# Performance work log

Measured on AMD Instinct MI355X. Metric: run time of the kernel, lower is better.

## Reference

```python
import jax, jax.numpy as jnp
import numpy as np

B, F, H, M, T = 4096, 256, 256, 3, 30
IN0 = 2 + F  # GRU layer-0 input: concat(current_pos[2], context[F])


def setup_inputs() -> dict:
    key = jax.random.key(0)
    ks = jax.random.split(key, 15)
    s = 0.05
    rn = lambda k, shp: jax.random.normal(k, shp, jnp.float32) * s
    return dict(
        context=jax.random.normal(ks[0], (B, F), jnp.float32),
        mp_w1=rn(ks[1], (64, F)), mp_b1=rn(ks[2], (64,)),
        mp_w2=rn(ks[3], (M, 64)), mp_b2=rn(ks[4], (M,)),
        w_ih0=rn(ks[5], (M, 3 * H, IN0)), w_hh0=rn(ks[6], (M, 3 * H, H)),
        b_ih0=rn(ks[7], (M, 3 * H)), b_hh0=rn(ks[8], (M, 3 * H)),
        w_ih1=rn(ks[9], (M, 3 * H, H)), w_hh1=rn(ks[10], (M, 3 * H, H)),
        b_ih1=rn(ks[11], (M, 3 * H)), b_hh1=rn(ks[12], (M, 3 * H)),
        out_w=rn(ks[13], (M, 2, H)), out_b=rn(ks[14], (M, 2)),
        num_future_steps=T,
    )


def _gru_cell(x, h, w_ih, w_hh, b_ih, b_hh):
    # PyTorch GRU cell, gate order (r, z, n)
    gx = x @ w_ih.T + b_ih  # (B, 3H)
    gh = h @ w_hh.T + b_hh  # (B, 3H)
    xr, xz, xn = jnp.split(gx, 3, axis=-1)
    hr, hz, hn = jnp.split(gh, 3, axis=-1)
    r = jax.nn.sigmoid(xr + hr)
    z = jax.nn.sigmoid(xz + hz)
    n = jnp.tanh(xn + r * hn)
    return (1.0 - z) * n + z * h


def reference(context, mp_w1, mp_b1, mp_w2, mp_b2,
              w_ih0, w_hh0, b_ih0, b_hh0,
              w_ih1, w_hh1, b_ih1, b_hh1,
              out_w, out_b, num_future_steps):
    mode_logits = jax.nn.relu(context @ mp_w1.T + mp_b1) @ mp_w2.T + mp_b2
    mode_probs = jax.nn.softmax(mode_logits, axis=-1)  # (B, M)

    def decode_mode(wi0, wh0, bi0, bh0, wi1, wh1, bi1, bh1, ow, ob):
        def step(carry, _):
            h0, h1, pos = carry
            x = jnp.concatenate([pos, context], axis=-1)  # (B, 2+F)
            h0n = _gru_cell(x, h0, wi0, wh0, bi0, bh0)
            h1n = _gru_cell(h0n, h1, wi1, wh1, bi1, bh1)
            delta = h1n @ ow.T + ob  # (B, 2)
            return (h0n, h1n, delta), delta

        pos0 = jnp.zeros((context.shape[0], 2), context.dtype)
        # hidden = context.unsqueeze(0).repeat(2,1,1): both layers init to context
        (_, _, _), deltas = jax.lax.scan(step, (context, context, pos0), None,
                                          length=num_future_steps)
        # deltas: (T, B, 2) -> (B, T, 2), cumulative sum over time
        return jnp.cumsum(deltas.transpose(1, 0, 2), axis=1)

    trajs = jax.vmap(decode_mode)(w_ih0, w_hh0, b_ih0, b_hh0,
                                  w_ih1, w_hh1, b_ih1, b_hh1,
                                  out_w, out_b)  # (M, B, T, 2)
    trajectories = trajs.transpose(1, 0, 2, 3)  # (B, M, T, 2)
    return trajectories, mode_probs
```

## Files before the change

kernel.cpp:

```cpp
#include <hip/hip_runtime.h>


typedef __attribute__((ext_vector_type(8))) short bf16x8;
typedef __attribute__((ext_vector_type(4))) short short4n;
typedef __attribute__((ext_vector_type(4))) float f32x4;

__device__ __forceinline__ short f2bf(float f) {
    unsigned u = __builtin_bit_cast(unsigned, f);
    unsigned r = (u + 0x7fffu + ((u >> 16) & 1u)) >> 16;
    return (short)r;
}
__device__ __forceinline__ float bf2f(short s) {
    unsigned u = ((unsigned)(unsigned short)s) << 16;
    return __builtin_bit_cast(float, u);
}
__device__ __forceinline__ float fast_sigmoid(float x) {
    x = fminf(fmaxf(x, -30.f), 30.f);
    float e = __builtin_amdgcn_exp2f(x * -1.442695041f);
    return __builtin_amdgcn_rcpf(1.f + e);
}
__device__ __forceinline__ float fast_tanh(float x) {
    x = fminf(fmaxf(x, -15.f), 15.f);
    float e = __builtin_amdgcn_exp2f(x * -2.885390082f);
    return (1.f - e) * __builtin_amdgcn_rcpf(1.f + e);
}

__global__ void prep_kernel(const float* __restrict__ w_ih0,
                            const float* __restrict__ w_hh0,
                            const float* __restrict__ w_ih1,
                            const float* __restrict__ w_hh1,
                            short* __restrict__ ws) {
    int bid = blockIdx.x;
    int L = threadIdx.x;
    const float* src;
    int srcRowLen, colBase, m, w, ks, t;
    if (bid < 1152) {
        int idx = bid, mw = idx / 48, blk = idx % 48;
        m = mw / 8; w = mw % 8;
        if (blk < 32) { ks = blk >> 2; t = blk & 3; }
        else { int q = blk - 32; ks = q >> 1; t = 4 + (q & 1); }
        src = w_hh0 + (size_t)m * 768 * 256; srcRowLen = 256; colBase = 0;
    } else if (bid < 3456) {
        int idx = bid - 1152, mw = idx / 96, blk = idx % 96;
        m = mw / 8; w = mw % 8;
        int half;
        if (blk < 64) { half = blk >> 5; ks = (blk >> 2) & 7; t = blk & 3; }
        else { int q = blk - 64; half = q >> 4; ks = (q >> 1) & 7; t = 4 + (q & 1); }
        src = (half ? w_hh1 : w_ih1) + (size_t)m * 768 * 256;
        srcRowLen = 256; colBase = 0;
    } else {
        int idx = bid - 3456, mw = idx / 48, blk = idx % 48;
        m = mw / 8; w = mw % 8; ks = blk / 6; t = blk % 6;
        src = w_ih0 + (size_t)m * 768 * 258; srcRowLen = 258; colBase = 2;
    }
    int row = (t >> 1) * 256 + 32 * w + (t & 1) * 16 + (L & 15);
    int col0 = colBase + ks * 32 + (L >> 4) * 8;
    short* dst = ws + (size_t)bid * 512 + L * 8;
    const float* s = src + (size_t)row * srcRowLen + col0;
#pragma unroll
    for (int j = 0; j < 8; ++j) dst[j] = f2bf(s[j]);
}

__global__ __launch_bounds__(256) void modeprobs_kernel(
    const float* __restrict__ ctx, const float* __restrict__ w1,
    const float* __restrict__ b1, const float* __restrict__ w2,
    const float* __restrict__ b2, float* __restrict__ out,
    long probs_off) {
    __shared__ float w1s[64 * 256];
    int tid = threadIdx.x;
    int j = tid & 63;
    int rsub = tid >> 6;
#pragma unroll
    for (int i = 0; i < 64; ++i) w1s[tid + i * 256] = w1[tid + i * 256];
    float b1v = b1[j];
    float w2v0 = w2[j], w2v1 = w2[64 + j], w2v2 = w2[128 + j];
    float b20 = b2[0], b21 = b2[1], b22 = b2[2];
    __syncthreads();
    for (int c = 0; c < 16; ++c) {
        int brow = blockIdx.x * 64 + c * 4 + rsub;
        const float* crow = ctx + (size_t)brow * 256;
        float accv = b1v;
#pragma unroll 8
        for (int k = 0; k < 256; ++k) {
            int kk = (k + j) & 255;
            accv += w1s[j * 256 + kk] * crow[kk];
        }
        float h = fmaxf(accv, 0.f);
        float l0 = h * w2v0, l1 = h * w2v1, l2 = h * w2v2;
#pragma unroll
        for (int s = 1; s < 64; s <<= 1) {
            l0 += __shfl_xor(l0, s);
            l1 += __shfl_xor(l1, s);
            l2 += __shfl_xor(l2, s);
        }
        if (j == 0) {
            l0 += b20; l1 += b21; l2 += b22;
            float mx = fmaxf(l0, fmaxf(l1, l2));
            float e0 = __builtin_amdgcn_exp2f((l0 - mx) * 1.442695041f);
            float e1 = __builtin_amdgcn_exp2f((l1 - mx) * 1.442695041f);
            float e2 = __builtin_amdgcn_exp2f((l2 - mx) * 1.442695041f);
            float inv = 1.f / (e0 + e1 + e2);
            out[probs_off + (size_t)brow * 3 + 0] = e0 * inv;
            out[probs_off + (size_t)brow * 3 + 1] = e1 * inv;
            out[probs_off + (size_t)brow * 3 + 2] = e2 * inv;
        }
    }
}

__global__ __launch_bounds__(512, 2) void decoder_gxc2(
    const float* __restrict__ context,
    const float* __restrict__ w_ih0_f,
    const float* __restrict__ b_ih0, const float* __restrict__ b_hh0,
    const float* __restrict__ b_ih1, const float* __restrict__ b_hh1,
    const float* __restrict__ out_w, const float* __restrict__ out_b,
    short* ws, float* __restrict__ out,
    const int* __restrict__ pT, int ntiles) {
    __shared__ short h0s[64 * 264];
    __shared__ short h1s[64 * 264];
    __shared__ short gxcrz[8 * 16 * 256];
    __shared__ float posD[128];
    __shared__ float owl[512];
    __shared__ short cwp0h[768], cwp1h[768];
    __shared__ float cbA[512];
    __shared__ float cbXn[256];
    __shared__ float cbh0n[256];
    __shared__ float cb1A[512];
    __shared__ float cb1X[256];
    __shared__ float cb1H[256];

    const int bid = blockIdx.x;
    const int xcd = bid & 7, slot = bid >> 3;
    int mode, xl, nx;
    if (xcd < 3)      { mode = 0; xl = xcd;     nx = 3; }
    else if (xcd < 6) { mode = 1; xl = xcd - 3; nx = 3; }
    else              { mode = 2; xl = xcd - 6; nx = 2; }
    const int g = slot * nx + xl;
    if (g >= ntiles) return;
    const int m = mode;
    const int b0 = g * 64;
    const int wk = m * ntiles + g;

    const int T = *pT;
    const int tid = threadIdx.x;
    const int lane = tid & 63, w = tid >> 6;
    const int lr = lane & 15, quad = lane >> 4;

    if (tid < 128) posD[tid] = 0.f;
    owl[tid] = out_w[m * 512 + tid];
    if (tid < 512) {
        cbA[tid] = b_ih0[m * 768 + tid] + b_hh0[m * 768 + tid];
        cb1A[tid] = b_ih1[m * 768 + tid] + b_hh1[m * 768 + tid];
    }
    if (tid < 256) {
        cbXn[tid] = b_ih0[m * 768 + 512 + tid];
        cbh0n[tid] = b_hh0[m * 768 + 512 + tid];
        cb1X[tid] = b_ih1[m * 768 + 512 + tid];
        cb1H[tid] = b_hh1[m * 768 + 512 + tid];
    }
    for (int cc = tid; cc < 768; cc += 512) {
        cwp0h[cc] = f2bf(w_ih0_f[((size_t)m * 768 + cc) * 258 + 0]);
        cwp1h[cc] = f2bf(w_ih0_f[((size_t)m * 768 + cc) * 258 + 1]);
    }
#pragma unroll
    for (int i = 0; i < 32; ++i) {
        int idx = tid + i * 512;
        int r = idx >> 8, k = idx & 255;
        short v = f2bf(context[(size_t)(b0 + r) * 256 + k]);
        h0s[r * 264 + k] = v;
        h1s[r * 264 + k] = v;
    }
    const float ob0v = out_b[m * 2 + 0], ob1v = out_b[m * 2 + 1];

    const short* p0w = ws + ((size_t)(m * 8 + w) * 48) * 512 + lane * 8;
    const short* p1w = ws + (size_t)1152 * 512 + ((size_t)(m * 8 + w) * 96) * 512 + lane * 8;
    const short* pcw = ws + (size_t)3456 * 512 + ((size_t)(m * 8 + w) * 48) * 512 + lane * 8;

    short* gxw = ws + (size_t)4608 * 512 +
                 ((size_t)(wk * 8 + w) * 8) * 256 + lane * 4;
    short* grz = gxcrz + (w * 16) * 256 + lane * 4;

    const int cA = 32 * w + lr;
    const int cB = 32 * w + 16 + lr;

    __syncthreads();

    {
        f32x4 arz[4][4], axn[2][4];
#pragma unroll
        for (int rt = 0; rt < 4; ++rt)
#pragma unroll
            for (int r = 0; r < 4; ++r) {
#pragma unroll
                for (int t = 0; t < 4; ++t) {
                    int c = (t >> 1) * 256 + ((t & 1) ? cB : cA);
                    arz[t][rt][r] = cbA[c];
                }
#pragma unroll
                for (int nt = 0; nt < 2; ++nt)
                    axn[nt][rt][r] = cbXn[nt ? cB : cA];
            }
        const short* bpc = pcw;
#pragma unroll 1
        for (int ks = 0; ks < 8; ++ks) {
            bf16x8 ac[4];
#pragma unroll
            for (int rt = 0; rt < 4; ++rt)
                ac[rt] = *reinterpret_cast<const bf16x8*>(
                    h0s + (rt * 16 + lr) * 264 + ks * 32 + quad * 8);
#pragma unroll
            for (int t = 0; t < 4; ++t) {
                bf16x8 b = *reinterpret_cast<const bf16x8*>(bpc + t * 512);
#pragma unroll
                for (int rt = 0; rt < 4; ++rt)
                    arz[t][rt] = __builtin_amdgcn_mfma_f32_16x16x32_bf16(
                        ac[rt], b, arz[t][rt], 0, 0, 0);
            }
#pragma unroll
            for (int nt = 0; nt < 2; ++nt) {
                bf16x8 b = *reinterpret_cast<const bf16x8*>(bpc + (4 + nt) * 512);
#pragma unroll
                for (int rt = 0; rt < 4; ++rt)
                    axn[nt][rt] = __builtin_amdgcn_mfma_f32_16x16x32_bf16(
                        ac[rt], b, axn[nt][rt], 0, 0, 0);
            }
            bpc += 6 * 512;
        }
#pragma unroll
        for (int t = 0; t < 4; ++t)
#pragma unroll
            for (int rt = 0; rt < 4; ++rt) {
                short4n pk;
#pragma unroll
                for (int r = 0; r < 4; ++r) pk[r] = f2bf(arz[t][rt][r]);
                *reinterpret_cast<short4n*>(grz + (t * 4 + rt) * 256) = pk;
            }
#pragma unroll
        for (int nt = 0; nt < 2; ++nt)
#pragma unroll
            for (int rt = 0; rt < 4; ++rt) {
                short4n pk;
#pragma unroll
                for (int r = 0; r < 4; ++r) pk[r] = f2bf(axn[nt][rt][r]);
                *reinterpret_cast<short4n*>(gxw + (nt * 4 + rt) * 256) = pk;
            }
        asm volatile("s_waitcnt vmcnt(0)" ::: "memory");
    }
    __syncthreads();

    float cum0 = 0.f, cum1 = 0.f;

    for (int st = 0; st < T; ++st) {
        {
            int gxo = 0;
            asm volatile("" : "+v"(gxo));
            const short* gq = gxw + gxo;

            f32x4 arz[4][4], axn[2][4], ahn[2][4];
#pragma unroll
            for (int t = 0; t < 4; ++t) {
                const int c = (t >> 1) * 256 + ((t & 1) ? cB : cA);
                const float w0 = bf2f(cwp0h[c]), w1 = bf2f(cwp1h[c]);
#pragma unroll
                for (int rt = 0; rt < 4; ++rt) {
                    short4n v = *reinterpret_cast<const short4n*>(
                        grz + (t * 4 + rt) * 256);
#pragma unroll
                    for (int r = 0; r < 4; ++r) {
                        int row = rt * 16 + quad * 4 + r;
                        arz[t][rt][r] = bf2f(v[r]) + posD[row * 2] * w0 +
                                        posD[row * 2 + 1] * w1;
                    }
                }
            }
#pragma unroll
            for (int nt = 0; nt < 2; ++nt) {
                const int cn = nt ? cB : cA;
                const float w0 = bf2f(cwp0h[512 + cn]);
                const float w1 = bf2f(cwp1h[512 + cn]);
                const float bh = cbh0n[cn];
#pragma unroll
                for (int rt = 0; rt < 4; ++rt) {
                    short4n v = *reinterpret_cast<const short4n*>(
                        gq + (nt * 4 + rt) * 256);
#pragma unroll
                    for (int r = 0; r < 4; ++r) {
                        int row = rt * 16 + quad * 4 + r;
                        axn[nt][rt][r] = bf2f(v[r]) + posD[row * 2] * w0 +
                                         posD[row * 2 + 1] * w1;
                        ahn[nt][rt][r] = bh;
                    }
                }
            }
            const short* b0r = p0w;
            const short* b0n = p0w + 32 * 512;
#pragma unroll 1
            for (int ks = 0; ks < 8; ++ks) {
                bf16x8 ah[4];
#pragma unroll
                for (int rt = 0; rt < 4; ++rt)
                    ah[rt] = *reinterpret_cast<const bf16x8*>(
                        h0s + (rt * 16 + lr) * 264 + ks * 32 + quad * 8);
#pragma unroll
                for (int t = 0; t < 4; ++t) {
                    bf16x8 b = *reinterpret_cast<const bf16x8*>(b0r + t * 512);
#pragma unroll
                    for (int rt = 0; rt < 4; ++rt)
                        arz[t][rt] = __builtin_amdgcn_mfma_f32_16x16x32_bf16(
                            ah[rt], b, arz[t][rt], 0, 0, 0);
                }
#pragma unroll
                for (int nt = 0; nt < 2; ++nt) {
                    bf16x8 b = *reinterpret_cast<const bf16x8*>(b0n + nt * 512);
#pragma unroll
                    for (int rt = 0; rt < 4; ++rt)
                        ahn[nt][rt] = __builtin_amdgcn_mfma_f32_16x16x32_bf16(
                            ah[rt], b, ahn[nt][rt], 0, 0, 0);
                }
                b0r += 4 * 512;
                b0n += 2 * 512;
            }
            __syncthreads();
#pragma unroll
            for (int nt = 0; nt < 2; ++nt) {
                int col = nt ? cB : cA;
#pragma unroll
                for (int rt = 0; rt < 4; ++rt)
#pragma unroll
                    for (int r = 0; r < 4; ++r) {
                        int row = rt * 16 + quad * 4 + r;
                        float rr = fast_sigmoid(arz[nt][rt][r]);
                        float zz = fast_sigmoid(arz[2 + nt][rt][r]);
                        float nn =
                            fast_tanh(axn[nt][rt][r] + rr * ahn[nt][rt][r]);
                        float hold = bf2f(h0s[row * 264 + col]);
                        h0s[row * 264 + col] = f2bf((1.f - zz) * nn + zz * hold);
                    }
            }
        }
        __syncthreads();

        {
            f32x4 arz[4][4], axn[2][4], ahn[2][4];
#pragma unroll
            for (int rt = 0; rt < 4; ++rt)
#pragma unroll
                for (int r = 0; r < 4; ++r) {
#pragma unroll
                    for (int t = 0; t < 4; ++t) {
                        int c = (t >> 1) * 256 + ((t & 1) ? cB : cA);
                        arz[t][rt][r] = cb1A[c];
                    }
#pragma unroll
                    for (int nt = 0; nt < 2; ++nt) {
                        int cn = nt ? cB : cA;
                        axn[nt][rt][r] = cb1X[cn];
                        ahn[nt][rt][r] = cb1H[cn];
                    }
                }
            const short* bq0 = p1w;
            const short* bq1 = p1w + 32 * 512;
            const short* bx = p1w + 64 * 512;
            const short* bh = p1w + 80 * 512;
#pragma unroll 1
            for (int ks = 0; ks < 8; ++ks) {
                bf16x8 a0[4], a1[4];
#pragma unroll
                for (int rt = 0; rt < 4; ++rt) {
                    a0[rt] = *reinterpret_cast<const bf16x8*>(
                        h0s + (rt * 16 + lr) * 264 + ks * 32 + quad * 8);
                    a1[rt] = *reinterpret_cast<const bf16x8*>(
                        h1s + (rt * 16 + lr) * 264 + ks * 32 + quad * 8);
                }
#pragma unroll
                for (int t = 0; t < 4; ++t) {
                    bf16x8 b = *reinterpret_cast<const bf16x8*>(bq0 + t * 512);
#pragma unroll
                    for (int rt = 0; rt < 4; ++rt)
                        arz[t][rt] = __builtin_amdgcn_mfma_f32_16x16x32_bf16(
                            a0[rt], b, arz[t][rt], 0, 0, 0);
                }
#pragma unroll
                for (int nt = 0; nt < 2; ++nt) {
                    bf16x8 b = *reinterpret_cast<const bf16x8*>(bx + nt * 512);
#pragma unroll
                    for (int rt = 0; rt < 4; ++rt)
                        axn[nt][rt] = __builtin_amdgcn_mfma_f32_16x16x32_bf16(
                            a0[rt], b, axn[nt][rt], 0, 0, 0);
                }
#pragma unroll
                for (int t = 0; t < 4; ++t) {
                    bf16x8 b = *reinterpret_cast<const bf16x8*>(bq1 + t * 512);
#pragma unroll
                    for (int rt = 0; rt < 4; ++rt)
                        arz[t][rt] = __builtin_amdgcn_mfma_f32_16x16x32_bf16(
                            a1[rt], b, arz[t][rt], 0, 0, 0);
                }
#pragma unroll
                for (int nt = 0; nt < 2; ++nt) {
                    bf16x8 b = *reinterpret_cast<const bf16x8*>(bh + nt * 512);
#pragma unroll
                    for (int rt = 0; rt < 4; ++rt)
                        ahn[nt][rt] = __builtin_amdgcn_mfma_f32_16x16x32_bf16(
                            a1[rt], b, ahn[nt][rt], 0, 0, 0);
                }
                bq0 += 4 * 512;
                bq1 += 4 * 512;
                bx += 2 * 512;
                bh += 2 * 512;
            }
            __syncthreads();
#pragma unroll
            for (int nt = 0; nt < 2; ++nt) {
                int col = nt ? cB : cA;
#pragma unroll
                for (int rt = 0; rt < 4; ++rt)
#pragma unroll
                    for (int r = 0; r < 4; ++r) {
                        int row = rt * 16 + quad * 4 + r;
                        float rr = fast_sigmoid(arz[nt][rt][r]);
                        float zz = fast_sigmoid(arz[2 + nt][rt][r]);
                        float nn =
                            fast_tanh(axn[nt][rt][r] + rr * ahn[nt][rt][r]);
                        float hold = bf2f(h1s[row * 264 + col]);
                        h1s[row * 264 + col] = f2bf((1.f - zz) * nn + zz * hold);
                    }
            }
        }
        __syncthreads();

        {
            int brow = tid >> 3, p = tid & 7;
            float d0 = 0.f, d1 = 0.f;
#pragma unroll
            for (int j = 0; j < 4; ++j) {
                int cb = ((p + brow) & 7) * 8 + j * 64;
                bf16x8 hv8 = *reinterpret_cast<const bf16x8*>(h1s + brow * 264 + cb);
#pragma unroll
                for (int i = 0; i < 8; ++i) {
                    float hv = bf2f(hv8[i]);
                    d0 += hv * owl[cb + i];
                    d1 += hv * owl[256 + cb + i];
                }
            }
            d0 += __shfl_xor(d0, 1); d0 += __shfl_xor(d0, 2); d0 += __shfl_xor(d0, 4);
            d1 += __shfl_xor(d1, 1); d1 += __shfl_xor(d1, 2); d1 += __shfl_xor(d1, 4);
            d0 += ob0v;
            d1 += ob1v;
            if (p == 0) {
                cum0 += d0;
                cum1 += d1;
                size_t o = (((size_t)(b0 + brow) * 3 + m) * (size_t)T + st) * 2;
                out[o] = cum0;
                out[o + 1] = cum1;
                posD[brow * 2] = d0;
                posD[brow * 2 + 1] = d1;
            }
        }
        __syncthreads();
    }
}

__global__ __launch_bounds__(512, 2) void decoder_base(
    const float* __restrict__ context,
    const float* __restrict__ w_ih0_f,
    const float* __restrict__ b_ih0, const float* __restrict__ b_hh0,
    const float* __restrict__ b_ih1, const float* __restrict__ b_hh1,
    const float* __restrict__ out_w, const float* __restrict__ out_b,
    const short* __restrict__ ws, float* __restrict__ out,
    const int* __restrict__ pT, int ntiles) {
    __shared__ short ctxS[64 * 264];
    __shared__ short h0a[64 * 264], h0b[64 * 264];
    __shared__ short h1s[64 * 264];
    __shared__ float posD[128];
    __shared__ float owl[512];
    __shared__ float cwp0[768], cwp1[768];
    __shared__ float cbA[512];
    __shared__ float cbXn[256];
    __shared__ float cbh0n[256];
    __shared__ float cb1A[512];
    __shared__ float cb1X[256];
    __shared__ float cb1H[256];

    const int bid = blockIdx.x;
    const int xcd = bid & 7, slot = bid >> 3;
    int mode, xl, nx;
    if (xcd < 3)      { mode = 0; xl = xcd;     nx = 3; }
    else if (xcd < 6) { mode = 1; xl = xcd - 3; nx = 3; }
    else              { mode = 2; xl = xcd - 6; nx = 2; }
    const int g = slot * nx + xl;
    if (g >= ntiles) return;
    const int m = mode;
    const int b0 = g * 64;

    const int T = *pT;
    const int tid = threadIdx.x;
    const int lane = tid & 63, w = tid >> 6;
    const int lr = lane & 15, quad = lane >> 4;

    if (tid < 128) posD[tid] = 0.f;
    owl[tid] = out_w[m * 512 + tid];
    if (tid < 512) {
        cbA[tid] = b_ih0[m * 768 + tid] + b_hh0[m * 768 + tid];
        cb1A[tid] = b_ih1[m * 768 + tid] + b_hh1[m * 768 + tid];
    }
    if (tid < 256) {
        cbXn[tid] = b_ih0[m * 768 + 512 + tid];
        cbh0n[tid] = b_hh0[m * 768 + 512 + tid];
        cb1X[tid] = b_ih1[m * 768 + 512 + tid];
        cb1H[tid] = b_hh1[m * 768 + 512 + tid];
    }
    for (int c = tid; c < 768; c += 512) {
        cwp0[c] = w_ih0_f[((size_t)m * 768 + c) * 258 + 0];
        cwp1[c] = w_ih0_f[((size_t)m * 768 + c) * 258 + 1];
    }
#pragma unroll
    for (int i = 0; i < 32; ++i) {
        int idx = tid + i * 512;
        int r = idx >> 8, k = idx & 255;
        short v = f2bf(context[(size_t)(b0 + r) * 256 + k]);
        ctxS[r * 264 + k] = v;
        h0a[r * 264 + k] = v;
        h1s[r * 264 + k] = v;
    }
    const float ob0v = out_b[m * 2 + 0], ob1v = out_b[m * 2 + 1];

    const short* p0w = ws + ((size_t)(m * 8 + w) * 48) * 512 + lane * 8;
    const short* p1w = ws + (size_t)1152 * 512 + ((size_t)(m * 8 + w) * 96) * 512 + lane * 8;
    const short* pcw = ws + (size_t)3456 * 512 + ((size_t)(m * 8 + w) * 48) * 512 + lane * 8;

    const int cA = 32 * w + lr;
    const int cB = 32 * w + 16 + lr;

    __syncthreads();

    float cum0 = 0.f, cum1 = 0.f;

    for (int st = 0; st < T; ++st) {
        const short* h0c = (st & 1) ? h0b : h0a;
        short* h0n_ = (st & 1) ? h0a : h0b;

        {
            f32x4 arz[4][4], axn[2][4], ahn[2][4];
#pragma unroll
            for (int rt = 0; rt < 4; ++rt)
#pragma unroll
                for (int r = 0; r < 4; ++r) {
                    int row = rt * 16 + quad * 4 + r;
                    float px = posD[row * 2], py = posD[row * 2 + 1];
#pragma unroll
                    for (int t = 0; t < 4; ++t) {
                        int c = (t >> 1) * 256 + ((t & 1) ? cB : cA);
                        arz[t][rt][r] = cbA[c] + px * cwp0[c] + py * cwp1[c];
                    }
#pragma unroll
                    for (int nt = 0; nt < 2; ++nt) {
                        int cn = nt ? cB : cA;
                        axn[nt][rt][r] = cbXn[cn] + px * cwp0[512 + cn] +
                                         py * cwp1[512 + cn];
                        ahn[nt][rt][r] = cbh0n[cn];
                    }
                }
            const short* bpc = pcw;
            const short* bp0rz = p0w;
            const short* bp0n = p0w + 32 * 512;
#pragma unroll 1
            for (int ks = 0; ks < 8; ++ks) {
                bf16x8 ac[4], ah[4];
#pragma unroll
                for (int rt = 0; rt < 4; ++rt) {
                    ac[rt] = *reinterpret_cast<const bf16x8*>(
                        ctxS + (rt * 16 + lr) * 264 + ks * 32 + quad * 8);
                    ah[rt] = *reinterpret_cast<const bf16x8*>(
                        h0c + (rt * 16 + lr) * 264 + ks * 32 + quad * 8);
                }
#pragma unroll
                for (int t = 0; t < 4; ++t) {
                    bf16x8 b = *reinterpret_cast<const bf16x8*>(bpc + t * 512);
#pragma unroll
                    for (int rt = 0; rt < 4; ++rt)
                        arz[t][rt] = __builtin_amdgcn_mfma_f32_16x16x32_bf16(
                            ac[rt], b, arz[t][rt], 0, 0, 0);
                }
#pragma unroll
                for (int nt = 0; nt < 2; ++nt) {
                    bf16x8 b = *reinterpret_cast<const bf16x8*>(bpc + (4 + nt) * 512);
#pragma unroll
                    for (int rt = 0; rt < 4; ++rt)
                        axn[nt][rt] = __builtin_amdgcn_mfma_f32_16x16x32_bf16(
                            ac[rt], b, axn[nt][rt], 0, 0, 0);
                }
#pragma unroll
                for (int t = 0; t < 4; ++t) {
                    bf16x8 b = *reinterpret_cast<const bf16x8*>(bp0rz + t * 512);
#pragma unroll
                    for (int rt = 0; rt < 4; ++rt)
                        arz[t][rt] = __builtin_amdgcn_mfma_f32_16x16x32_bf16(
                            ah[rt], b, arz[t][rt], 0, 0, 0);
                }
#pragma unroll
                for (int nt = 0; nt < 2; ++nt) {
                    bf16x8 b = *reinterpret_cast<const bf16x8*>(bp0n + nt * 512);
#pragma unroll
                    for (int rt = 0; rt < 4; ++rt)
                        ahn[nt][rt] = __builtin_amdgcn_mfma_f32_16x16x32_bf16(
                            ah[rt], b, ahn[nt][rt], 0, 0, 0);
                }
                bpc += 6 * 512;
                bp0rz += 4 * 512;
                bp0n += 2 * 512;
            }
#pragma unroll
            for (int nt = 0; nt < 2; ++nt) {
                int col = nt ? cB : cA;
#pragma unroll
                for (int rt = 0; rt < 4; ++rt)
#pragma unroll
                    for (int r = 0; r < 4; ++r) {
                        int row = rt * 16 + quad * 4 + r;
                        float rr = fast_sigmoid(arz[nt][rt][r]);
                        float zz = fast_sigmoid(arz[2 + nt][rt][r]);
                        float nn =
                            fast_tanh(axn[nt][rt][r] + rr * ahn[nt][rt][r]);
                        float hold = bf2f(h0c[row * 264 + col]);
                        h0n_[row * 264 + col] = f2bf((1.f - zz) * nn + zz * hold);
                    }
            }
        }
        __syncthreads();

        {
            f32x4 arz[4][4], axn[2][4], ahn[2][4];
#pragma unroll
            for (int rt = 0; rt < 4; ++rt)
#pragma unroll
                for (int r = 0; r < 4; ++r) {
#pragma unroll
                    for (int t = 0; t < 4; ++t) {
                        int c = (t >> 1) * 256 + ((t & 1) ? cB : cA);
                        arz[t][rt][r] = cb1A[c];
                    }
#pragma unroll
                    for (int nt = 0; nt < 2; ++nt) {
                        int cn = nt ? cB : cA;
                        axn[nt][rt][r] = cb1X[cn];
                        ahn[nt][rt][r] = cb1H[cn];
                    }
                }
            const short* bq0 = p1w;
            const short* bq1 = p1w + 32 * 512;
            const short* bx = p1w + 64 * 512;
            const short* bh = p1w + 80 * 512;
#pragma unroll 1
            for (int ks = 0; ks < 8; ++ks) {
                bf16x8 a0[4], a1[4];
#pragma unroll
                for (int rt = 0; rt < 4; ++rt) {
                    a0[rt] = *reinterpret_cast<const bf16x8*>(
                        h0n_ + (rt * 16 + lr) * 264 + ks * 32 + quad * 8);
                    a1[rt] = *reinterpret_cast<const bf16x8*>(
                        h1s + (rt * 16 + lr) * 264 + ks * 32 + quad * 8);
                }
#pragma unroll
                for (int t = 0; t < 4; ++t) {
                    bf16x8 b = *reinterpret_cast<const bf16x8*>(bq0 + t * 512);
#pragma unroll
                    for (int rt = 0; rt < 4; ++rt)
                        arz[t][rt] = __builtin_amdgcn_mfma_f32_16x16x32_bf16(
                            a0[rt], b, arz[t][rt], 0, 0, 0);
                }
#pragma unroll
                for (int nt = 0; nt < 2; ++nt) {
                    bf16x8 b = *reinterpret_cast<const bf16x8*>(bx + nt * 512);
#pragma unroll
                    for (int rt = 0; rt < 4; ++rt)
                        axn[nt][rt] = __builtin_amdgcn_mfma_f32_16x16x32_bf16(
                            a0[rt], b, axn[nt][rt], 0, 0, 0);
                }
#pragma unroll
                for (int t = 0; t < 4; ++t) {
                    bf16x8 b = *reinterpret_cast<const bf16x8*>(bq1 + t * 512);
#pragma unroll
                    for (int rt = 0; rt < 4; ++rt)
                        arz[t][rt] = __builtin_amdgcn_mfma_f32_16x16x32_bf16(
                            a1[rt], b, arz[t][rt], 0, 0, 0);
                }
#pragma unroll
                for (int nt = 0; nt < 2; ++nt) {
                    bf16x8 b = *reinterpret_cast<const bf16x8*>(bh + nt * 512);
#pragma unroll
                    for (int rt = 0; rt < 4; ++rt)
                        ahn[nt][rt] = __builtin_amdgcn_mfma_f32_16x16x32_bf16(
                            a1[rt], b, ahn[nt][rt], 0, 0, 0);
                }
                bq0 += 4 * 512;
                bq1 += 4 * 512;
                bx += 2 * 512;
                bh += 2 * 512;
            }
            __syncthreads();
#pragma unroll
            for (int nt = 0; nt < 2; ++nt) {
                int col = nt ? cB : cA;
#pragma unroll
                for (int rt = 0; rt < 4; ++rt)
#pragma unroll
                    for (int r = 0; r < 4; ++r) {
                        int row = rt * 16 + quad * 4 + r;
                        float rr = fast_sigmoid(arz[nt][rt][r]);
                        float zz = fast_sigmoid(arz[2 + nt][rt][r]);
                        float nn =
                            fast_tanh(axn[nt][rt][r] + rr * ahn[nt][rt][r]);
                        float hold = bf2f(h1s[row * 264 + col]);
                        h1s[row * 264 + col] = f2bf((1.f - zz) * nn + zz * hold);
                    }
            }
        }
        __syncthreads();

        {
            int brow = tid >> 3, p = tid & 7;
            float d0 = 0.f, d1 = 0.f;
#pragma unroll
            for (int j = 0; j < 4; ++j) {
                int cb = ((p + brow) & 7) * 8 + j * 64;
                bf16x8 hv8 = *reinterpret_cast<const bf16x8*>(h1s + brow * 264 + cb);
#pragma unroll
                for (int i = 0; i < 8; ++i) {
                    float hv = bf2f(hv8[i]);
                    d0 += hv * owl[cb + i];
                    d1 += hv * owl[256 + cb + i];
                }
            }
            d0 += __shfl_xor(d0, 1); d0 += __shfl_xor(d0, 2); d0 += __shfl_xor(d0, 4);
            d1 += __shfl_xor(d1, 1); d1 += __shfl_xor(d1, 2); d1 += __shfl_xor(d1, 4);
            d0 += ob0v;
            d1 += ob1v;
            if (p == 0) {
                cum0 += d0;
                cum1 += d1;
                size_t o = (((size_t)(b0 + brow) * 3 + m) * (size_t)T + st) * 2;
                out[o] = cum0;
                out[o + 1] = cum1;
                posD[brow * 2] = d0;
                posD[brow * 2 + 1] = d1;
            }
        }
        __syncthreads();
    }
}

extern "C" void kernel_launch(void* const* d_in, const int* in_sizes, int n_in,
                              void* d_out, int out_size, void* d_ws, size_t ws_size,
                              hipStream_t stream) {
    const float* context = (const float*)d_in[0];
    const float* mp_w1 = (const float*)d_in[1];
    const float* mp_b1 = (const float*)d_in[2];
    const float* mp_w2 = (const float*)d_in[3];
    const float* mp_b2 = (const float*)d_in[4];
    const float* w_ih0 = (const float*)d_in[5];
    const float* w_hh0 = (const float*)d_in[6];
    const float* b_ih0 = (const float*)d_in[7];
    const float* b_hh0 = (const float*)d_in[8];
    const float* w_ih1 = (const float*)d_in[9];
    const float* w_hh1 = (const float*)d_in[10];
    const float* b_ih1 = (const float*)d_in[11];
    const float* b_hh1 = (const float*)d_in[12];
    const float* out_w = (const float*)d_in[13];
    const float* out_b = (const float*)d_in[14];
    const int* pT = (const int*)d_in[15];
    float* out = (float*)d_out;
    short* ws = (short*)d_ws;

    const int B = in_sizes[0] / 256;
    const int ntiles = B / 64;
    const long probs_off = (long)out_size - (long)B * 3;

    prep_kernel<<<4608, 64, 0, stream>>>(w_ih0, w_hh0, w_ih1, w_hh1, ws);
    modeprobs_kernel<<<B / 64, 256, 0, stream>>>(context, mp_w1, mp_b1, mp_w2,
                                                 mp_b2, out, probs_off);
    const int nslots = (ntiles + 1) / 2;

    const size_t needed =
        ((size_t)4608 * 512 + (size_t)3 * ntiles * 8 * 8 * 256) * sizeof(short);
    if (ws_size >= needed) {
        decoder_gxc2<<<8 * nslots, 512, 0, stream>>>(
            context, w_ih0, b_ih0, b_hh0, b_ih1, b_hh1, out_w, out_b, ws, out,
            pT, ntiles);
    } else {
        decoder_base<<<8 * nslots, 512, 0, stream>>>(
            context, w_ih0, b_ih0, b_hh0, b_ih1, b_hh1, out_w, out_b, ws, out,
            pT, ntiles);
    }
}
```

Measured before the change: 876.2 us.

## Split decoder into 32-row tiles with 256-thread blocks, two column groups per wave

The decoder moves from 64-row batch tiles with 8 waves to 32-row tiles with 4 waves, each wave now handling two 32-column gate groups. Work items (mode, tile) are assigned to blocks contiguously per XCD lane, replacing the hard-coded mode-to-XCD mapping. This doubles the block count (384 vs 192), which should fill more CUs on a 256-CU part and cut the length of the serial recurrence chain per block. In exchange, each weight fragment is reused across fewer rows, so per-block weight traffic relative to useful work roughly doubles, and register pressure per wave rises.

```diff
diff --git a/kernel.cpp b/kernel.cpp
--- a/kernel.cpp
+++ b/kernel.cpp
@@ -107,18 +107,18 @@
     }
 }
 
-__global__ __launch_bounds__(512, 2) void decoder_gxc2(
+__global__ __launch_bounds__(256, 2) void decoder_gxc32(
     const float* __restrict__ context,
     const float* __restrict__ w_ih0_f,
     const float* __restrict__ b_ih0, const float* __restrict__ b_hh0,
     const float* __restrict__ b_ih1, const float* __restrict__ b_hh1,
     const float* __restrict__ out_w, const float* __restrict__ out_b,
     short* ws, float* __restrict__ out,
-    const int* __restrict__ pT, int ntiles) {
-    __shared__ short h0s[64 * 264];
-    __shared__ short h1s[64 * 264];
-    __shared__ short gxcrz[8 * 16 * 256];
-    __shared__ float posD[128];
+    const int* __restrict__ pT, int tilesPerMode, int nwork) {
+    __shared__ short h0s[32 * 264];
+    __shared__ short h1s[32 * 264];
+    __shared__ short gxcrz[8 * 8 * 256];
+    __shared__ float posD[64];
     __shared__ float owl[512];
     __shared__ short cwp0h[768], cwp1h[768];
     __shared__ float cbA[512];
@@ -128,121 +128,139 @@
     __shared__ float cb1X[256];
     __shared__ float cb1H[256];
 
-    const int bid = blockIdx.x;
-    const int xcd = bid & 7, slot = bid >> 3;
-    int mode, xl, nx;
-    if (xcd < 3)      { mode = 0; xl = xcd;     nx = 3; }
-    else if (xcd < 6) { mode = 1; xl = xcd - 3; nx = 3; }
-    else              { mode = 2; xl = xcd - 6; nx = 2; }
-    const int g = slot * nx + xl;
-    if (g >= ntiles) return;
-    const int m = mode;
-    const int b0 = g * 64;
-    const int wk = m * ntiles + g;
+    const int lane8 = blockIdx.x & 7, slot = blockIdx.x >> 3;
+    const int q = nwork >> 3, r8 = nwork & 7;
+    int start, cnt;
+    if (lane8 < r8) { cnt = q + 1; start = lane8 * (q + 1); }
+    else            { cnt = q;     start = r8 * (q + 1) + (lane8 - r8) * q; }
+    if (slot >= cnt) return;
+    const int wk = start + slot;
+    const int m = wk / tilesPerMode;
+    const int b0 = (wk - m * tilesPerMode) * 32;
 
     const int T = *pT;
     const int tid = threadIdx.x;
     const int lane = tid & 63, w = tid >> 6;
     const int lr = lane & 15, quad = lane >> 4;
 
-    if (tid < 128) posD[tid] = 0.f;
+    if (tid < 64) posD[tid] = 0.f;
     owl[tid] = out_w[m * 512 + tid];
-    if (tid < 512) {
-        cbA[tid] = b_ih0[m * 768 + tid] + b_hh0[m * 768 + tid];
-        cb1A[tid] = b_ih1[m * 768 + tid] + b_hh1[m * 768 + tid];
-    }
-    if (tid < 256) {
-        cbXn[tid] = b_ih0[m * 768 + 512 + tid];
-        cbh0n[tid] = b_hh0[m * 768 + 512 + tid];
-        cb1X[tid] = b_ih1[m * 768 + 512 + tid];
-        cb1H[tid] = b_hh1[m * 768 + 512 + tid];
-    }
-    for (int cc = tid; cc < 768; cc += 512) {
+    owl[256 + tid] = out_w[m * 512 + 256 + tid];
+    cbA[tid] = b_ih0[m * 768 + tid] + b_hh0[m * 768 + tid];
+    cbA[256 + tid] = b_ih0[m * 768 + 256 + tid] + b_hh0[m * 768 + 256 + tid];
+    cb1A[tid] = b_ih1[m * 768 + tid] + b_hh1[m * 768 + tid];
+    cb1A[256 + tid] = b_ih1[m * 768 + 256 + tid] + b_hh1[m * 768 + 256 + tid];
+    cbXn[tid] = b_ih0[m * 768 + 512 + tid];
+    cbh0n[tid] = b_hh0[m * 768 + 512 + tid];
+    cb1X[tid] = b_ih1[m * 768 + 512 + tid];
+    cb1H[tid] = b_hh1[m * 768 + 512 + tid];
+    for (int cc = tid; cc < 768; cc += 256) {
         cwp0h[cc] = f2bf(w_ih0_f[((size_t)m * 768 + cc) * 258 + 0]);
         cwp1h[cc] = f2bf(w_ih0_f[((size_t)m * 768 + cc) * 258 + 1]);
     }
 #pragma unroll
     for (int i = 0; i < 32; ++i) {
-        int idx = tid + i * 512;
-        int r = idx >> 8, k = idx & 255;
-        short v = f2bf(context[(size_t)(b0 + r) * 256 + k]);
-        h0s[r * 264 + k] = v;
-        h1s[r * 264 + k] = v;
+        int idx = tid + i * 256;
+        int rr = idx >> 8, k = idx & 255;
+        short v = f2bf(context[(size_t)(b0 + rr) * 256 + k]);
+        h0s[rr * 264 + k] = v;
+        h1s[rr * 264 + k] = v;
     }
     const float ob0v = out_b[m * 2 + 0], ob1v = out_b[m * 2 + 1];
 
-    const short* p0w = ws + ((size_t)(m * 8 + w) * 48) * 512 + lane * 8;
-    const short* p1w = ws + (size_t)1152 * 512 + ((size_t)(m * 8 + w) * 96) * 512 + lane * 8;
-    const short* pcw = ws + (size_t)3456 * 512 + ((size_t)(m * 8 + w) * 48) * 512 + lane * 8;
-
-    short* gxw = ws + (size_t)4608 * 512 +
-                 ((size_t)(wk * 8 + w) * 8) * 256 + lane * 4;
-    short* grz = gxcrz + (w * 16) * 256 + lane * 4;
-
-    const int cA = 32 * w + lr;
-    const int cB = 32 * w + 16 + lr;
+    const short* p0B[2];
+    const short* p1B[2];
+    const short* pcB[2];
+    short* gxB[2];
+#pragma unroll
+    for (int g2 = 0; g2 < 2; ++g2) {
+        const int wg = 2 * w + g2;
+        p0B[g2] = ws + ((size_t)(m * 8 + wg) * 48) * 512 + lane * 8;
+        p1B[g2] = ws + (size_t)1152 * 512 + ((size_t)(m * 8 + wg) * 96) * 512 + lane * 8;
+        pcB[g2] = ws + (size_t)3456 * 512 + ((size_t)(m * 8 + wg) * 48) * 512 + lane * 8;
+        gxB[g2] = ws + (size_t)4608 * 512 +
+                  ((size_t)(wk * 8 + wg) * 4) * 256 + lane * 4;
+    }
 
     __syncthreads();
 
     {
-        f32x4 arz[4][4], axn[2][4];
-#pragma unroll
-        for (int rt = 0; rt < 4; ++rt)
-#pragma unroll
-            for (int r = 0; r < 4; ++r) {
-#pragma unroll
-                for (int t = 0; t < 4; ++t) {
-                    int c = (t >> 1) * 256 + ((t & 1) ? cB : cA);
-                    arz[t][rt][r] = cbA[c];
-                }
-#pragma unroll
-                for (int nt = 0; nt < 2; ++nt)
-                    axn[nt][rt][r] = cbXn[nt ? cB : cA];
-            }
-        const short* bpc = pcw;
+        f32x4 arz[2][4][2], axn[2][2][2];
+#pragma unroll
+        for (int g2 = 0; g2 < 2; ++g2) {
+            const int cbase = 32 * (2 * w + g2) + lr;
+#pragma unroll
+            for (int t = 0; t < 4; ++t) {
+                const int c = (t >> 1) * 256 + cbase + (t & 1) * 16;
+                const float bb = cbA[c];
+#pragma unroll
+                for (int rt = 0; rt < 2; ++rt)
+#pragma unroll
+                    for (int r = 0; r < 4; ++r) arz[g2][t][rt][r] = bb;
+            }
+#pragma unroll
+            for (int nt = 0; nt < 2; ++nt) {
+                const float bx = cbXn[cbase + nt * 16];
+#pragma unroll
+                for (int rt = 0; rt < 2; ++rt)
+#pragma unroll
+                    for (int r = 0; r < 4; ++r) axn[g2][nt][rt][r] = bx;
+            }
+        }
+        const short* bpc0 = pcB[0];
+        const short* bpc1 = pcB[1];
 #pragma unroll 1
         for (int ks = 0; ks < 8; ++ks) {
-            bf16x8 ac[4];
-#pragma unroll
-            for (int rt = 0; rt < 4; ++rt)
+            bf16x8 ac[2];
+#pragma unroll
+            for (int rt = 0; rt < 2; ++rt)
                 ac[rt] = *reinterpret_cast<const bf16x8*>(
                     h0s + (rt * 16 + lr) * 264 + ks * 32 + quad * 8);
 #pragma unroll
-            for (int t = 0; t < 4; ++t) {
-                bf16x8 b = *reinterpret_cast<const bf16x8*>(bpc + t * 512);
-#pragma unroll
-                for (int rt = 0; rt < 4; ++rt)
-                    arz[t][rt] = __builtin_amdgcn_mfma_f32_16x16x32_bf16(
-                        ac[rt], b, arz[t][rt], 0, 0, 0);
-            }
-#pragma unroll
-            for (int nt = 0; nt < 2; ++nt) {
-                bf16x8 b = *reinterpret_cast<const bf16x8*>(bpc + (4 + nt) * 512);
-#pragma unroll
-                for (int rt = 0; rt < 4; ++rt)
-                    axn[nt][rt] = __builtin_amdgcn_mfma_f32_16x16x32_bf16(
-                        ac[rt], b, axn[nt][rt], 0, 0, 0);
-            }
-            bpc += 6 * 512;
-        }
-#pragma unroll
-        for (int t = 0; t < 4; ++t)
-#pragma unroll
-            for (int rt = 0; rt < 4; ++rt) {
-                short4n pk;
-#pragma unroll
-                for (int r = 0; r < 4; ++r) pk[r] = f2bf(arz[t][rt][r]);
-                *reinterpret_cast<short4n*>(grz + (t * 4 + rt) * 256) = pk;
-            }
-#pragma unroll
-        for (int nt = 0; nt < 2; ++nt)
-#pragma unroll
-            for (int rt = 0; rt < 4; ++rt) {
-                short4n pk;
-#pragma unroll
-                for (int r = 0; r < 4; ++r) pk[r] = f2bf(axn[nt][rt][r]);
-                *reinterpret_cast<short4n*>(gxw + (nt * 4 + rt) * 256) = pk;
-            }
+            for (int g2 = 0; g2 < 2; ++g2) {
+                const short* bpc = g2 ? bpc1 : bpc0;
+#pragma unroll
+                for (int t = 0; t < 4; ++t) {
+                    bf16x8 b = *reinterpret_cast<const bf16x8*>(bpc + t * 512);
+#pragma unroll
+                    for (int rt = 0; rt < 2; ++rt)
+                        arz[g2][t][rt] = __builtin_amdgcn_mfma_f32_16x16x32_bf16(
+                            ac[rt], b, arz[g2][t][rt], 0, 0, 0);
+                }
+#pragma unroll
+                for (int nt = 0; nt < 2; ++nt) {
+                    bf16x8 b = *reinterpret_cast<const bf16x8*>(bpc + (4 + nt) * 512);
+#pragma unroll
+                    for (int rt = 0; rt < 2; ++rt)
+                        axn[g2][nt][rt] = __builtin_amdgcn_mfma_f32_16x16x32_bf16(
+                            ac[rt], b, axn[g2][nt][rt], 0, 0, 0);
+                }
+            }
+            bpc0 += 6 * 512;
+            bpc1 += 6 * 512;
+        }
+#pragma unroll
+        for (int g2 = 0; g2 < 2; ++g2) {
+            short* grz = gxcrz + ((2 * w + g2) * 8) * 256 + lane * 4;
+#pragma unroll
+            for (int t = 0; t < 4; ++t)
+#pragma unroll
+                for (int rt = 0; rt < 2; ++rt) {
+                    short4n pk;
+#pragma unroll
+                    for (int r = 0; r < 4; ++r) pk[r] = f2bf(arz[g2][t][rt][r]);
+                    *reinterpret_cast<short4n*>(grz + (t * 2 + rt) * 256) = pk;
+                }
+#pragma unroll
+            for (int nt = 0; nt < 2; ++nt)
+#pragma unroll
+                for (int rt = 0; rt < 2; ++rt) {
+                    short4n pk;
+#pragma unroll
+                    for (int r = 0; r < 4; ++r) pk[r] = f2bf(axn[g2][nt][rt][r]);
+                    *reinterpret_cast<short4n*>(gxB[g2] + (nt * 2 + rt) * 256) = pk;
+                }
+        }
         asm volatile("s_waitcnt vmcnt(0)" ::: "memory");
     }
     __syncthreads();
@@ -253,178 +271,223 @@
         {
             int gxo = 0;
             asm volatile("" : "+v"(gxo));
-            const short* gq = gxw + gxo;
-
-            f32x4 arz[4][4], axn[2][4], ahn[2][4];
-#pragma unroll
-            for (int t = 0; t < 4; ++t) {
-                const int c = (t >> 1) * 256 + ((t & 1) ? cB : cA);
-                const float w0 = bf2f(cwp0h[c]), w1 = bf2f(cwp1h[c]);
-#pragma unroll
-                for (int rt = 0; rt < 4; ++rt) {
-                    short4n v = *reinterpret_cast<const short4n*>(
-                        grz + (t * 4 + rt) * 256);
-#pragma unroll
-                    for (int r = 0; r < 4; ++r) {
-                        int row = rt * 16 + quad * 4 + r;
-                        arz[t][rt][r] = bf2f(v[r]) + posD[row * 2] * w0 +
-                                        posD[row * 2 + 1] * w1;
-                    }
-                }
-            }
-#pragma unroll
-            for (int nt = 0; nt < 2; ++nt) {
-                const int cn = nt ? cB : cA;
-                const float w0 = bf2f(cwp0h[512 + cn]);
-                const float w1 = bf2f(cwp1h[512 + cn]);
-                const float bh = cbh0n[cn];
-#pragma unroll
-                for (int rt = 0; rt < 4; ++rt) {
-                    short4n v = *reinterpret_cast<const short4n*>(
-                        gq + (nt * 4 + rt) * 256);
-#pragma unroll
-                    for (int r = 0; r < 4; ++r) {
-                        int row = rt * 16 + quad * 4 + r;
-                        axn[nt][rt][r] = bf2f(v[r]) + posD[row * 2] * w0 +
-                                         posD[row * 2 + 1] * w1;
-                        ahn[nt][rt][r] = bh;
-                    }
-                }
-            }
-            const short* b0r = p0w;
-            const short* b0n = p0w + 32 * 512;
+
+            f32x4 arz[2][4][2], axn[2][2][2], ahn[2][2][2];
+            float px[2][4], py[2][4];
+#pragma unroll
+            for (int rt = 0; rt < 2; ++rt)
+#pragma unroll
+                for (int rr = 0; rr < 4; ++rr) {
+                    int row = rt * 16 + quad * 4 + rr;
+                    px[rt][rr] = posD[row * 2];
+                    py[rt][rr] = posD[row * 2 + 1];
+                }
+#pragma unroll
+            for (int g2 = 0; g2 < 2; ++g2) {
+                const int cbase = 32 * (2 * w + g2) + lr;
+                const short* grz = gxcrz + ((2 * w + g2) * 8) * 256 + lane * 4;
+                const short* gq = gxB[g2] + gxo;
+#pragma unroll
+                for (int t = 0; t < 4; ++t) {
+                    const int c = (t >> 1) * 256 + cbase + (t & 1) * 16;
+                    const float w0 = bf2f(cwp0h[c]), w1 = bf2f(cwp1h[c]);
+#pragma unroll
+                    for (int rt = 0; rt < 2; ++rt) {
+                        short4n v = *reinterpret_cast<const short4n*>(
+                            grz + (t * 2 + rt) * 256);
+#pragma unroll
+                        for (int r = 0; r < 4; ++r)
+                            arz[g2][t][rt][r] = bf2f(v[r]) + px[rt][r] * w0 +
+                                                py[rt][r] * w1;
+                    }
+                }
+#pragma unroll
+                for (int nt = 0; nt < 2; ++nt) {
+                    const int cn = cbase + nt * 16;
+                    const float w0 = bf2f(cwp0h[512 + cn]);
+                    const float w1 = bf2f(cwp1h[512 + cn]);
+                    const float bh = cbh0n[cn];
+#pragma unroll
+                    for (int rt = 0; rt < 2; ++rt) {
+                        short4n v = *reinterpret_cast<const short4n*>(
+                            gq + (nt * 2 + rt) * 256);
+#pragma unroll
+                        for (int r = 0; r < 4; ++r) {
+                            axn[g2][nt][rt][r] = bf2f(v[r]) + px[rt][r] * w0 +
+                                                 py[rt][r] * w1;
+                            ahn[g2][nt][rt][r] = bh;
+                        }
+                    }
+                }
+            }
+            const short* brz0 = p0B[0];
+            const short* brz1 = p0B[1];
+            const short* bn0 = p0B[0] + 32 * 512;
+            const short* bn1 = p0B[1] + 32 * 512;
 #pragma unroll 1
             for (int ks = 0; ks < 8; ++ks) {
-                bf16x8 ah[4];
-#pragma unroll
-                for (int rt = 0; rt < 4; ++rt)
+                bf16x8 ah[2];
+#pragma unroll
+                for (int rt = 0; rt < 2; ++rt)
                     ah[rt] = *reinterpret_cast<const bf16x8*>(
                         h0s + (rt * 16 + lr) * 264 + ks * 32 + quad * 8);
 #pragma unroll
+                for (int g2 = 0; g2 < 2; ++g2) {
+                    const short* brz = g2 ? brz1 : brz0;
+                    const short* bn = g2 ? bn1 : bn0;
+#pragma unroll
+                    for (int t = 0; t < 4; ++t) {
+                        bf16x8 b = *reinterpret_cast<const bf16x8*>(brz + t * 512);
+#pragma unroll
+                        for (int rt = 0; rt < 2; ++rt)
+                            arz[g2][t][rt] = __builtin_amdgcn_mfma_f32_16x16x32_bf16(
+                                ah[rt], b, arz[g2][t][rt], 0, 0, 0);
+                    }
+#pragma unroll
+                    for (int nt = 0; nt < 2; ++nt) {
+                        bf16x8 b = *reinterpret_cast<const bf16x8*>(bn + nt * 512);
+#pragma unroll
+                        for (int rt = 0; rt < 2; ++rt)
+                            ahn[g2][nt][rt] = __builtin_amdgcn_mfma_f32_16x16x32_bf16(
+                                ah[rt], b, ahn[g2][nt][rt], 0, 0, 0);
+                    }
+                }
+                brz0 += 4 * 512; brz1 += 4 * 512;
+                bn0 += 2 * 512;  bn1 += 2 * 512;
+            }
+            __syncthreads();
+#pragma unroll
+            for (int g2 = 0; g2 < 2; ++g2)
+#pragma unroll
+                for (int nt = 0; nt < 2; ++nt) {
+                    const int col = 32 * (2 * w + g2) + nt * 16 + lr;
+#pragma unroll
+                    for (int rt = 0; rt < 2; ++rt)
+#pragma unroll
+                        for (int rr = 0; rr < 4; ++rr) {
+                            int row = rt * 16 + quad * 4 + rr;
+                            float rg = fast_sigmoid(arz[g2][nt][rt][rr]);
+                            float zg = fast_sigmoid(arz[g2][2 + nt][rt][rr]);
+                            float ng = fast_tanh(axn[g2][nt][rt][rr] +
+                                                 rg * ahn[g2][nt][rt][rr]);
+                            float hold = bf2f(h0s[row * 264 + col]);
+                            h0s[row * 264 + col] =
+                                f2bf((1.f - zg) * ng + zg * hold);
+                        }
+                }
+        }
+        __syncthreads();
+
+        {
+            f32x4 arz[2][4][2], axn[2][2][2], ahn[2][2][2];
+#pragma unroll
+            for (int g2 = 0; g2 < 2; ++g2) {
+                const int cbase = 32 * (2 * w + g2) + lr;
+#pragma unroll
                 for (int t = 0; t < 4; ++t) {
-                    bf16x8 b = *reinterpret_cast<const bf16x8*>(b0r + t * 512);
-#pragma unroll
-                    for (int rt = 0; rt < 4; ++rt)
-                        arz[t][rt] = __builtin_amdgcn_mfma_f32_16x16x32_bf16(
-                            ah[rt], b, arz[t][rt], 0, 0, 0);
+                    const int c = (t >> 1) * 256 + cbase + (t & 1) * 16;
+                    const float bb = cb1A[c];
+#pragma unroll
+                    for (int rt = 0; rt < 2; ++rt)
+#pragma unroll
+                        for (int rr = 0; rr < 4; ++rr)
+                            arz[g2][t][rt][rr] = bb;
                 }
 #pragma unroll
                 for (int nt = 0; nt < 2; ++nt) {
-                    bf16x8 b = *reinterpret_cast<const bf16x8*>(b0n + nt * 512);
-#pragma unroll
-                    for (int rt = 0; rt < 4; ++rt)
-                        ahn[nt][rt] = __builtin_amdgcn_mfma_f32_16x16x32_bf16(
-                            ah[rt], b, ahn[nt][rt], 0, 0, 0);
-                }
-                b0r += 4 * 512;
-                b0n += 2 * 512;
-            }
-            __syncthreads();
-#pragma unroll
-            for (int nt = 0; nt < 2; ++nt) {
-                int col = nt ? cB : cA;
-#pragma unroll
-                for (int rt = 0; rt < 4; ++rt)
-#pragma unroll
-                    for (int r = 0; r < 4; ++r) {
-                        int row = rt * 16 + quad * 4 + r;
-                        float rr = fast_sigmoid(arz[nt][rt][r]);
-                        float zz = fast_sigmoid(arz[2 + nt][rt][r]);
-                        float nn =
-                            fast_tanh(axn[nt][rt][r] + rr * ahn[nt][rt][r]);
-                        float hold = bf2f(h0s[row * 264 + col]);
-                        h0s[row * 264 + col] = f2bf((1.f - zz) * nn + zz * hold);
-                    }
-            }
-        }
-        __syncthreads();
-
-        {
-            f32x4 arz[4][4], axn[2][4], ahn[2][4];
-#pragma unroll
-            for (int rt = 0; rt < 4; ++rt)
-#pragma unroll
-                for (int r = 0; r < 4; ++r) {
-#pragma unroll
-                    for (int t = 0; t < 4; ++t) {
-                        int c = (t >> 1) * 256 + ((t & 1) ? cB : cA);
-                        arz[t][rt][r] = cb1A[c];
-                    }
-#pragma unroll
-                    for (int nt = 0; nt < 2; ++nt) {
-                        int cn = nt ? cB : cA;
-                        axn[nt][rt][r] = cb1X[cn];
-                        ahn[nt][rt][r] = cb1H[cn];
-                    }
-                }
-            const short* bq0 = p1w;
-            const short* bq1 = p1w + 32 * 512;
-            const short* bx = p1w + 64 * 512;
-            const short* bh = p1w + 80 * 512;
+                    const int cn = cbase + nt * 16;
+                    const float bx = cb1X[cn], bh = cb1H[cn];
+#pragma unroll
+                    for (int rt = 0; rt < 2; ++rt)
+#pragma unroll
+                        for (int rr = 0; rr < 4; ++rr) {
+                            axn[g2][nt][rt][rr] = bx;
+                            ahn[g2][nt][rt][rr] = bh;
+                        }
+                }
+            }
+            const short* bq00 = p1B[0];
+            const short* bq01 = p1B[1];
+            const short* bq10 = p1B[0] + 32 * 512;
+            const short* bq11 = p1B[1] + 32 * 512;
+            const short* bx0 = p1B[0] + 64 * 512;
+            const short* bx1 = p1B[1] + 64 * 512;
+            const short* bh0 = p1B[0] + 80 * 512;
+            const short* bh1 = p1B[1] + 80 * 512;
 #pragma unroll 1
             for (int ks = 0; ks < 8; ++ks) {
-                bf16x8 a0[4], a1[4];
-#pragma unroll
-                for (int rt = 0; rt < 4; ++rt) {
+                bf16x8 a0[2], a1[2];
+#pragma unroll
+                for (int rt = 0; rt < 2; ++rt) {
                     a0[rt] = *reinterpret_cast<const bf16x8*>(
                         h0s + (rt * 16 + lr) * 264 + ks * 32 + quad * 8);
                     a1[rt] = *reinterpret_cast<const bf16x8*>(
                         h1s + (rt * 16 + lr) * 264 + ks * 32 + quad * 8);
                 }
 #pragma unroll
-                for (int t = 0; t < 4; ++t) {
-                    bf16x8 b = *reinterpret_cast<const bf16x8*>(bq0 + t * 512);
-#pragma unroll
-                    for (int rt = 0; rt < 4; ++rt)
-                        arz[t][rt] = __builtin_amdgcn_mfma_f32_16x16x32_bf16(
-                            a0[rt], b, arz[t][rt], 0, 0, 0);
-                }
+                for (int g2 = 0; g2 < 2; ++g2) {
+                    const short* bq0 = g2 ? bq01 : bq00;
+                    const short* bq1 = g2 ? bq11 : bq10;
+                    const short* bxp = g2 ? bx1 : bx0;
+                    const short* bhp = g2 ? bh1 : bh0;
+#pragma unroll
+                    for (int t = 0; t < 4; ++t) {
+                        bf16x8 b = *reinterpret_cast<const bf16x8*>(bq0 + t * 512);
+#pragma unroll
+                        for (int rt = 0; rt < 2; ++rt)
+                            arz[g2][t][rt] = __builtin_amdgcn_mfma_f32_16x16x32_bf16(
+                                a0[rt], b, arz[g2][t][rt], 0, 0, 0);
+                    }
+#pragma unroll
+                    for (int nt = 0; nt < 2; ++nt) {
+                        bf16x8 b = *reinterpret_cast<const bf16x8*>(bxp + nt * 512);
+#pragma unroll
+                        for (int rt = 0; rt < 2; ++rt)
+                            axn[g2][nt][rt] = __builtin_amdgcn_mfma_f32_16x16x32_bf16(
+                                a0[rt], b, axn[g2][nt][rt], 0, 0, 0);
+                    }
+#pragma unroll
+                    for (int t = 0; t < 4; ++t) {
+                        bf16x8 b = *reinterpret_cast<const bf16x8*>(bq1 + t * 512);
+#pragma unroll
+                        for (int rt = 0; rt < 2; ++rt)
+                            arz[g2][t][rt] = __builtin_amdgcn_mfma_f32_16x16x32_bf16(
+                                a1[rt], b, arz[g2][t][rt], 0, 0, 0);
+                    }
+#pragma unroll
+                    for (int nt = 0; nt < 2; ++nt) {
+                        bf16x8 b = *reinterpret_cast<const bf16x8*>(bhp + nt * 512);
+#pragma unroll
+                        for (int rt = 0; rt < 2; ++rt)
+                            ahn[g2][nt][rt] = __builtin_amdgcn_mfma_f32_16x16x32_bf16(
+                                a1[rt], b, ahn[g2][nt][rt], 0, 0, 0);
+                    }
+                }
+                bq00 += 4 * 512; bq01 += 4 * 512;
+                bq10 += 4 * 512; bq11 += 4 * 512;
+                bx0 += 2 * 512;  bx1 += 2 * 512;
+                bh0 += 2 * 512;  bh1 += 2 * 512;
+            }
+            __syncthreads();
+#pragma unroll
+            for (int g2 = 0; g2 < 2; ++g2)
 #pragma unroll
                 for (int nt = 0; nt < 2; ++nt) {
-                    bf16x8 b = *reinterpret_cast<const bf16x8*>(bx + nt * 512);
-#pragma unroll
-                    for (int rt = 0; rt < 4; ++rt)
-                        axn[nt][rt] = __builtin_amdgcn_mfma_f32_16x16x32_bf16(
-                            a0[rt], b, axn[nt][rt], 0, 0, 0);
-                }
-#pragma unroll
-                for (int t = 0; t < 4; ++t) {
-                    bf16x8 b = *reinterpret_cast<const bf16x8*>(bq1 + t * 512);
-#pragma unroll
-                    for (int rt = 0; rt < 4; ++rt)
-                        arz[t][rt] = __builtin_amdgcn_mfma_f32_16x16x32_bf16(
-                            a1[rt], b, arz[t][rt], 0, 0, 0);
-                }
-#pragma unroll
-                for (int nt = 0; nt < 2; ++nt) {
-                    bf16x8 b = *reinterpret_cast<const bf16x8*>(bh + nt * 512);
-#pragma unroll
-                    for (int rt = 0; rt < 4; ++rt)
-                        ahn[nt][rt] = __builtin_amdgcn_mfma_f32_16x16x32_bf16(
-                            a1[rt], b, ahn[nt][rt], 0, 0, 0);
-                }
-                bq0 += 4 * 512;
-                bq1 += 4 * 512;
-                bx += 2 * 512;
-                bh += 2 * 512;
-            }
-            __syncthreads();
-#pragma unroll
-            for (int nt = 0; nt < 2; ++nt) {
-                int col = nt ? cB : cA;
-#pragma unroll
-                for (int rt = 0; rt < 4; ++rt)
-#pragma unroll
-                    for (int r = 0; r < 4; ++r) {
-                        int row = rt * 16 + quad * 4 + r;
-                        float rr = fast_sigmoid(arz[nt][rt][r]);
-                        float zz = fast_sigmoid(arz[2 + nt][rt][r]);
-                        float nn =
-                            fast_tanh(axn[nt][rt][r] + rr * ahn[nt][rt][r]);
-                        float hold = bf2f(h1s[row * 264 + col]);
-                        h1s[row * 264 + col] = f2bf((1.f - zz) * nn + zz * hold);
-                    }
-            }
+                    const int col = 32 * (2 * w + g2) + nt * 16 + lr;
+#pragma unroll
+                    for (int rt = 0; rt < 2; ++rt)
+#pragma unroll
+                        for (int rr = 0; rr < 4; ++rr) {
+                            int row = rt * 16 + quad * 4 + rr;
+                            float rg = fast_sigmoid(arz[g2][nt][rt][rr]);
+                            float zg = fast_sigmoid(arz[g2][2 + nt][rt][rr]);
+                            float ng = fast_tanh(axn[g2][nt][rt][rr] +
+                                                 rg * ahn[g2][nt][rt][rr]);
+                            float hold = bf2f(h1s[row * 264 + col]);
+                            h1s[row * 264 + col] =
+                                f2bf((1.f - zg) * ng + zg * hold);
+                        }
+                }
         }
         __syncthreads();
 
@@ -772,21 +835,24 @@
     short* ws = (short*)d_ws;
 
     const int B = in_sizes[0] / 256;
-    const int ntiles = B / 64;
     const long probs_off = (long)out_size - (long)B * 3;
 
     prep_kernel<<<4608, 64, 0, stream>>>(w_ih0, w_hh0, w_ih1, w_hh1, ws);
     modeprobs_kernel<<<B / 64, 256, 0, stream>>>(context, mp_w1, mp_b1, mp_w2,
                                                  mp_b2, out, probs_off);
-    const int nslots = (ntiles + 1) / 2;
-
+
+    const int tilesPerMode = B / 32;
+    const int nwork = 3 * tilesPerMode;
     const size_t needed =
-        ((size_t)4608 * 512 + (size_t)3 * ntiles * 8 * 8 * 256) * sizeof(short);
+        ((size_t)4608 * 512 + (size_t)nwork * 8 * 4 * 256) * sizeof(short);
     if (ws_size >= needed) {
-        decoder_gxc2<<<8 * nslots, 512, 0, stream>>>(
+        const int grid = 8 * ((nwork + 7) / 8);
+        decoder_gxc32<<<grid, 256, 0, stream>>>(
             context, w_ih0, b_ih0, b_hh0, b_ih1, b_hh1, out_w, out_b, ws, out,
-            pT, ntiles);
+            pT, tilesPerMode, nwork);
     } else {
+        const int ntiles = B / 64;
+        const int nslots = (ntiles + 1) / 2;
         decoder_base<<<8 * nslots, 512, 0, stream>>>(
             context, w_ih0, b_ih0, b_hh0, b_ih1, b_hh1, out_w, out_b, ws, out,
             pT, ntiles);
```

New measurement: 1.003 ms. +14.4%, slower.
